# Kernel tuning notes

Hardware: AMD Instinct MI355X
Metric: run time of the kernel (lower is better)

The kernel has to match this reference:

```python
import jax, jax.numpy as jnp
import numpy as np

N_NODES = 100000
N_FEAT = 128
HIDDEN = 32
HEADS = 4
N_CLASSES = 40
N_EDGES = 1600000
NEG_SLOPE = 0.2


def gat_conv(x, src, dst, W, att_src, att_dst, bias):
    """PyG-style GATConv (concat=True, eval mode, self-loops already in src/dst).
    x: [N, Fin], W: [Fin, H*C], att_src/att_dst: [H, C], bias: [H*C].
    """
    N = x.shape[0]
    H, C = att_src.shape
    h = (x @ W).reshape(N, H, C)                       # [N, H, C]
    a_src = jnp.einsum('nhc,hc->nh', h, att_src)       # [N, H]
    a_dst = jnp.einsum('nhc,hc->nh', h, att_dst)       # [N, H]
    e = a_src[src] + a_dst[dst]                        # [E, H]
    e = jnp.where(e > 0, e, NEG_SLOPE * e)             # leaky_relu(0.2)
    # segment softmax over incoming edges of each destination node
    e_max = jax.ops.segment_max(e, dst, num_segments=N)
    e = jnp.exp(e - e_max[dst])
    denom = jax.ops.segment_sum(e, dst, num_segments=N)
    alpha = e / (denom[dst] + 1e-16)                   # [E, H]
    msg = alpha[:, :, None] * h[src]                   # [E, H, C]
    out = jax.ops.segment_sum(msg, dst, num_segments=N)  # [N, H, C]
    return out.reshape(N, H * C) + bias


def setup_inputs() -> dict:
    key = jax.random.key(0)
    ks = jax.random.split(key, 10)
    s = 0.1
    x = jax.random.normal(ks[0], (N_NODES, N_FEAT), dtype=jnp.float32)
    edge_index = jax.random.randint(ks[1], (2, N_EDGES), 0, N_NODES, dtype=jnp.int32)
    W1 = jax.random.normal(ks[2], (N_FEAT, HEADS * HIDDEN), dtype=jnp.float32) * s
    att_src1 = jax.random.normal(ks[3], (HEADS, HIDDEN), dtype=jnp.float32) * s
    att_dst1 = jax.random.normal(ks[4], (HEADS, HIDDEN), dtype=jnp.float32) * s
    b1 = jnp.zeros((HEADS * HIDDEN,), dtype=jnp.float32)
    W2 = jax.random.normal(ks[5], (HEADS * HIDDEN, HEADS * HIDDEN), dtype=jnp.float32) * s
    att_src2 = jax.random.normal(ks[6], (HEADS, HIDDEN), dtype=jnp.float32) * s
    att_dst2 = jax.random.normal(ks[7], (HEADS, HIDDEN), dtype=jnp.float32) * s
    b2 = jnp.zeros((HEADS * HIDDEN,), dtype=jnp.float32)
    Wc = jax.random.normal(ks[8], (HEADS * HIDDEN, N_CLASSES), dtype=jnp.float32) * s
    bc = jnp.zeros((N_CLASSES,), dtype=jnp.float32)
    return {"x": x, "edge_index": edge_index, "W1": W1, "att_src1": att_src1,
            "att_dst1": att_dst1, "b1": b1, "W2": W2, "att_src2": att_src2,
            "att_dst2": att_dst2, "b2": b2, "Wc": Wc, "bc": bc}


def reference(x, edge_index, W1, att_src1, att_dst1, b1, W2, att_src2, att_dst2, b2, Wc, bc):
    N = x.shape[0]
    loops = jnp.arange(N, dtype=edge_index.dtype)
    src = jnp.concatenate([edge_index[0], loops])  # PyG add_self_loops=True
    dst = jnp.concatenate([edge_index[1], loops])
    h = gat_conv(x, src, dst, W1, att_src1, att_dst1, b1)
    h = jax.nn.relu(h)  # dropout p=0.5 inactive in eval
    h = gat_conv(h, src, dst, W2, att_src2, att_dst2, b2)
    h = jax.nn.relu(h)  # dropout p=0.6 inactive in eval
    return h @ Wc + bc
```

## Files before the change

kernel.cpp:

```cpp
#include <hip/hip_runtime.h>

#define NN   100000
#define NE   1600000
#define BSH  9
#define BSZ  512
#define NBK  196
#define TA   4096
#define NBA  391
#define SCAP 64
#define CAP2 9216
#define NBG  782
#define NPREP 7

typedef _Float16 half_t;
typedef __attribute__((ext_vector_type(2))) _Float16 f16x2;
typedef __attribute__((ext_vector_type(4))) _Float16 f16x4;
typedef __attribute__((ext_vector_type(8))) _Float16 f16x8;
typedef __attribute__((ext_vector_type(4))) float    f32x4;

__global__ __launch_bounds__(256) void k_front(const float* __restrict__ X, const float* __restrict__ W1,
                                               const float* __restrict__ atts, const float* __restrict__ attd,
                                               half_t* __restrict__ H, float* __restrict__ asrc,
                                               float* __restrict__ adst,
                                               const float* __restrict__ W2, const float* __restrict__ Wc,
                                               const float* __restrict__ atts2, const float* __restrict__ attd2,
                                               half_t* __restrict__ WT2, half_t* __restrict__ WTc,
                                               const int* __restrict__ src, const int* __restrict__ dst,
                                               unsigned int* __restrict__ bpk, int* __restrict__ bh) {
  __shared__ __align__(16) char smem[21760];
  int t = threadIdx.x;
  int bid = blockIdx.x;

  if (bid >= NBG + NPREP) {
    int hb = bid - NBG - NPREP;
    int* hist  = (int*)smem;
    int* hscan = hist + NBK;
    int* cnt   = hscan + NBK;
    int* ssc   = cnt + NBK;
    unsigned int* staged = (unsigned int*)(ssc + 256);
    int e0 = hb * TA;
    if (t < NBK) { hist[t] = 0; cnt[t] = 0; }
    __syncthreads();
#pragma unroll
    for (int i = 0; i < TA / 256; i++) {
      int e = e0 + t + i * 256;
      if (e < NE) atomicAdd(&hist[dst[e] >> BSH], 1);
    }
    __syncthreads();
    {
      int v = (t < NBK) ? hist[t] : 0;
      int x = v;
      ssc[t] = x;
      for (int off = 1; off < 256; off <<= 1) {
        __syncthreads();
        int y = (t >= off) ? ssc[t - off] : 0;
        __syncthreads();
        x += y;
        ssc[t] = x;
      }
      if (t < NBK) hscan[t] = x - v;
    }
    __syncthreads();
#pragma unroll
    for (int i = 0; i < TA / 256; i++) {
      int e = e0 + t + i * 256;
      if (e < NE) {
        int d = dst[e];
        int bk = d >> BSH;
        int pos = hscan[bk] + atomicAdd(&cnt[bk], 1);
        staged[pos] = ((unsigned int)src[e] << BSH) | (unsigned int)(d & (BSZ - 1));
      }
    }
    __syncthreads();
    int wave = t >> 6, lane = t & 63;
    for (int bk = wave; bk < NBK; bk += 4) {
      int c = hist[bk];
      int cw = min(c, SCAP);
      size_t base = ((size_t)bk * NBA + hb) * SCAP;
      int lo = hscan[bk];
      for (int j = lane; j < cw; j += 64) bpk[base + j] = staged[lo + j];
      if (lane == 0) bh[bk * NBA + hb] = cw;
    }
    return;
  }

  if (bid >= NBG) {
    int b = bid - NBG;
    if (b == 6) {
      int e = t >> 5, kr = t & 31, h = e & 3;
      const float* att = ((e < 4) ? atts2 : attd2) + h * 32;
#pragma unroll
      for (int u = 0; u < 4; u++) {
        int k = u * 32 + kr;
        const float* wrow = W2 + (size_t)k * 128 + h * 32;
        float s = 0.f;
#pragma unroll
        for (int c = 0; c < 32; c += 4) {
          float4 wv = *(const float4*)(wrow + c);
          float4 av = *(const float4*)(att + c);
          s += wv.x * av.x + wv.y * av.y + wv.z * av.z + wv.w * av.w;
        }
        WT2[(size_t)(128 + e) * 128 + k] = (half_t)s;
      }
      for (int u = t; u < 8 * 128; u += 256) WT2[(size_t)136 * 128 + u] = (half_t)0.f;
      return;
    }
    float (*tile)[65] = (float(*)[65])smem;
    const float* W;
    half_t* WT;
    int k0, n0, N, NTr;
    if (b < 4) { W = W2; WT = WT2; k0 = (b >> 1) * 64; n0 = (b & 1) * 64; N = 128; NTr = 128; }
    else       { int bb = b - 4; W = Wc; WT = WTc; k0 = bb * 64; n0 = 0; N = 40; NTr = 48; }
    int col = t & 63, r4 = t >> 6;
#pragma unroll
    for (int i = 0; i < 16; i++) {
      int row = r4 * 16 + i;
      float v = 0.f;
      if (n0 + col < N) v = W[(size_t)(k0 + row) * N + n0 + col];
      tile[row][col] = v;
    }
    __syncthreads();
#pragma unroll
    for (int i = 0; i < 16; i++) {
      int nrow = r4 * 16 + i;
      if (n0 + nrow < NTr) WT[(size_t)(n0 + nrow) * 128 + k0 + col] = (half_t)tile[col][nrow];
    }
    return;
  }

  half_t* Xt = (half_t*)smem;
  half_t* Wt = Xt + 128 * 40;
  int wave = t >> 6, lane = t & 63;
  int l15 = lane & 15, quad = lane >> 4;
  int rb = bid * 128;

  for (int u = t; u < 8 * 40; u += 256) Wt[136 * 40 + u] = (half_t)0.f;

  f32x4 acc[2][9];
#pragma unroll
  for (int rt = 0; rt < 2; rt++)
#pragma unroll
    for (int ct = 0; ct < 9; ct++) acc[rt][ct] = (f32x4){0.f, 0.f, 0.f, 0.f};

  for (int k0 = 0; k0 < 128; k0 += 32) {
    __syncthreads();
#pragma unroll
    for (int i = 0; i < 4; i++) {
      int lin = i * 256 + t;
      int row = lin >> 3;
      int c4 = (lin & 7) * 4;
      float4 v = make_float4(0.f, 0.f, 0.f, 0.f);
      int gr = rb + row;
      if (gr < NN) v = *(const float4*)(X + (size_t)gr * 128 + k0 + c4);
      f16x4 hv;
      hv[0] = (half_t)v.x; hv[1] = (half_t)v.y; hv[2] = (half_t)v.z; hv[3] = (half_t)v.w;
      *(f16x4*)(Xt + row * 40 + c4) = hv;
    }
#pragma unroll
    for (int i = 0; i < 4; i++) {
      int lin = i * 256 + t;
      int kr = lin >> 5;
      int n4 = (lin & 31) * 4;
      float4 v = *(const float4*)(W1 + (size_t)(k0 + kr) * 128 + n4);
      Wt[(n4 + 0) * 40 + kr] = (half_t)v.x;
      Wt[(n4 + 1) * 40 + kr] = (half_t)v.y;
      Wt[(n4 + 2) * 40 + kr] = (half_t)v.z;
      Wt[(n4 + 3) * 40 + kr] = (half_t)v.w;
    }
    {
      int e = t >> 5, kr = t & 31, h = e & 3;
      const float* att = ((e < 4) ? atts : attd) + h * 32;
      const float* wrow = W1 + (size_t)(k0 + kr) * 128 + h * 32;
      float s = 0.f;
#pragma unroll
      for (int c = 0; c < 32; c += 4) {
        float4 wv = *(const float4*)(wrow + c);
        float4 av = *(const float4*)(att + c);
        s += wv.x * av.x + wv.y * av.y + wv.z * av.z + wv.w * av.w;
      }
      Wt[(128 + e) * 40 + kr] = (half_t)s;
    }
    __syncthreads();

    f16x8 a0 = *(const f16x8*)(Xt + (wave * 32 + l15) * 40 + quad * 8);
    f16x8 a1 = *(const f16x8*)(Xt + (wave * 32 + 16 + l15) * 40 + quad * 8);
#pragma unroll
    for (int ct = 0; ct < 9; ct++) {
      f16x8 b = *(const f16x8*)(Wt + (ct * 16 + l15) * 40 + quad * 8);
      acc[0][ct] = __builtin_amdgcn_mfma_f32_16x16x32_f16(a0, b, acc[0][ct], 0, 0, 0);
      acc[1][ct] = __builtin_amdgcn_mfma_f32_16x16x32_f16(a1, b, acc[1][ct], 0, 0, 0);
    }
  }

#pragma unroll
  for (int rt = 0; rt < 2; rt++) {
    int rbase = rb + wave * 32 + rt * 16 + quad * 4;
#pragma unroll
    for (int reg = 0; reg < 4; reg++) {
      int row = rbase + reg;
      if (row < NN) {
#pragma unroll
        for (int ct = 0; ct < 8; ct++) {
          H[(size_t)row * 128 + ct * 16 + l15] = (half_t)acc[rt][ct][reg];
        }
        if (l15 < 8) {
          float v = acc[rt][8][reg];
          if (l15 < 4) asrc[row * 4 + l15] = v;
          else         adst[row * 4 + (l15 - 4)] = v;
        }
      }
    }
  }
}

__global__ __launch_bounds__(256) void k_binB(const unsigned int* __restrict__ bpk,
                                              const int* __restrict__ bh,
                                              int* __restrict__ sbeg, int* __restrict__ send,
                                              int* __restrict__ adj) {
  __shared__ int lhist[BSZ];
  __shared__ int lscan[BSZ];
  __shared__ int lcur[BSZ];
  __shared__ int ssc[256];
  __shared__ int carr[NBA];
  __shared__ unsigned int staged[CAP2];
  int b = blockIdx.x;
  int t = threadIdx.x;
  int nbeg = b << BSH;
  int nloc = min(BSZ, NN - nbeg);
  int adjb = b * CAP2;
  for (int u = t; u < NBA; u += 256) carr[u] = bh[b * NBA + u];
  lhist[2 * t] = (2 * t < nloc) ? 1 : 0;
  lhist[2 * t + 1] = (2 * t + 1 < nloc) ? 1 : 0;
  lcur[2 * t] = 1;
  lcur[2 * t + 1] = 1;
  __syncthreads();
  int wave = t >> 6, lane = t & 63;
  for (int a = wave; a < NBA; a += 4) {
    int c = carr[a];
    size_t base = ((size_t)b * NBA + a) * SCAP;
    for (int j = lane; j < c; j += 64) atomicAdd(&lhist[bpk[base + j] & (BSZ - 1)], 1);
  }
  __syncthreads();
  {
    int v0 = lhist[2 * t], v1 = lhist[2 * t + 1];
    int s2 = v0 + v1;
    int x = s2;
    ssc[t] = x;
    for (int off = 1; off < 256; off <<= 1) {
      __syncthreads();
      int y = (t >= off) ? ssc[t - off] : 0;
      __syncthreads();
      x += y;
      ssc[t] = x;
    }
    int ex = x - s2;
    lscan[2 * t] = ex;
    lscan[2 * t + 1] = ex + v0;
  }
  __syncthreads();
  int total = lscan[BSZ - 1] + lhist[BSZ - 1];
#pragma unroll
  for (int u = 0; u < 2; u++) {
    int i = t + u * 256;
    if (i < nloc) {
      int bg = adjb + lscan[i];
      sbeg[nbeg + i] = bg;
      send[nbeg + i] = bg + lhist[i];
      staged[lscan[i]] = (unsigned int)(nbeg + i);
    }
  }
  __syncthreads();
  for (int a = wave; a < NBA; a += 4) {
    int c = carr[a];
    size_t base = ((size_t)b * NBA + a) * SCAP;
    for (int j = lane; j < c; j += 64) {
      unsigned int v = bpk[base + j];
      int dl = v & (BSZ - 1);
      int idx = lscan[dl] + atomicAdd(&lcur[dl], 1);
      if (idx < CAP2) staged[idx] = v >> BSH;
    }
  }
  __syncthreads();
  int lim = min(total, CAP2);
  for (int i = t; i < lim; i += 256) adj[adjb + i] = (int)staged[i];
}

__global__ __launch_bounds__(256) void k_agg(const half_t* __restrict__ H, const int* __restrict__ sbeg,
                                             const int* __restrict__ send, const int* __restrict__ adj,
                                             const float* __restrict__ asrc, const float* __restrict__ adst,
                                             const float* __restrict__ bias, half_t* __restrict__ out) {
  int n = blockIdx.x * 4 + (threadIdx.x >> 6);
  if (n >= NN) return;
  int lane = threadIdx.x & 63;
  int sub = lane & 7;
  int g = lane >> 3;
  int head = sub >> 1;
  float ad = adst[(size_t)n * 4 + head];
  float acc[16];
#pragma unroll
  for (int j = 0; j < 16; j++) acc[j] = 0.f;
  float wsum = 0.f;
  int beg = sbeg[n], end = send[n];
  int i = beg + g;
  int s = 0;
  float a = 0.f;
  if (i < end) {
    s = adj[i];
    a = asrc[(size_t)s * 4 + head];
  }
  while (i < end) {
    int inext = i + 8;
    int sn = 0;
    float an = 0.f;
    if (inext < end) {
      sn = adj[inext];
      an = asrc[(size_t)sn * 4 + head];
    }
    float ev = a + ad;
    ev = (ev > 0.f) ? ev : 0.2f * ev;
    float w = __expf(ev);
    const f16x8* hp = (const f16x8*)(H + (size_t)s * 128 + sub * 16);
    f16x8 h0 = hp[0], h1 = hp[1];
    wsum += w;
#pragma unroll
    for (int j = 0; j < 8; j++) acc[j] += w * (float)h0[j];
#pragma unroll
    for (int j = 0; j < 8; j++) acc[8 + j] += w * (float)h1[j];
    s = sn; a = an; i = inext;
  }
#pragma unroll
  for (int m = 8; m < 64; m <<= 1) {
    wsum += __shfl_xor(wsum, m, 64);
#pragma unroll
    for (int j = 0; j < 16; j++) acc[j] += __shfl_xor(acc[j], m, 64);
  }
  float scale = 1.0f / (wsum + 1e-16f);
  float o0 = acc[0], o1 = acc[1];
#pragma unroll
  for (int r = 1; r < 8; r++) {
    if (g == r) { o0 = acc[2 * r]; o1 = acc[2 * r + 1]; }
  }
  int ch = sub * 16 + g * 2;
  o0 = fmaxf(o0 * scale + bias[ch], 0.f);
  o1 = fmaxf(o1 * scale + bias[ch + 1], 0.f);
  f16x2 o;
  o[0] = (half_t)o0;
  o[1] = (half_t)o1;
  *(f16x2*)(out + (size_t)n * 128 + ch) = o;
}

__global__ __launch_bounds__(256) void k_gemm_att(const half_t* __restrict__ X, const half_t* __restrict__ WT,
                                                  half_t* __restrict__ H, float* __restrict__ asrc,
                                                  float* __restrict__ adst) {
  __shared__ __align__(16) half_t Xt[128 * 40];
  __shared__ __align__(16) half_t Wt[144 * 40];
  int t = threadIdx.x;
  int wave = t >> 6, lane = t & 63;
  int l15 = lane & 15, quad = lane >> 4;
  int rb = blockIdx.x * 128;

  f32x4 acc[2][9];
#pragma unroll
  for (int rt = 0; rt < 2; rt++)
#pragma unroll
    for (int ct = 0; ct < 9; ct++) acc[rt][ct] = (f32x4){0.f, 0.f, 0.f, 0.f};

  for (int k0 = 0; k0 < 128; k0 += 32) {
    __syncthreads();
#pragma unroll
    for (int i = 0; i < 2; i++) {
      int lin = i * 256 + t;
      int row = lin >> 2;
      int c8 = (lin & 3) * 8;
      f16x8 hv = (f16x8)(half_t)0;
      int gr = rb + row;
      if (gr < NN) hv = *(const f16x8*)(X + (size_t)gr * 128 + k0 + c8);
      *(f16x8*)(Xt + row * 40 + c8) = hv;
    }
#pragma unroll
    for (int i = 0; i < 3; i++) {
      int lin = i * 256 + t;
      if (lin < 576) {
        int row = lin >> 2;
        int c8 = (lin & 3) * 8;
        *(f16x8*)(Wt + row * 40 + c8) = *(const f16x8*)(WT + (size_t)row * 128 + k0 + c8);
      }
    }
    __syncthreads();

    f16x8 a0 = *(const f16x8*)(Xt + (wave * 32 + l15) * 40 + quad * 8);
    f16x8 a1 = *(const f16x8*)(Xt + (wave * 32 + 16 + l15) * 40 + quad * 8);
#pragma unroll
    for (int ct = 0; ct < 9; ct++) {
      f16x8 b = *(const f16x8*)(Wt + (ct * 16 + l15) * 40 + quad * 8);
      acc[0][ct] = __builtin_amdgcn_mfma_f32_16x16x32_f16(a0, b, acc[0][ct], 0, 0, 0);
      acc[1][ct] = __builtin_amdgcn_mfma_f32_16x16x32_f16(a1, b, acc[1][ct], 0, 0, 0);
    }
  }

#pragma unroll
  for (int rt = 0; rt < 2; rt++) {
    int rbase = rb + wave * 32 + rt * 16 + quad * 4;
#pragma unroll
    for (int reg = 0; reg < 4; reg++) {
      int row = rbase + reg;
      if (row < NN) {
#pragma unroll
        for (int ct = 0; ct < 8; ct++) {
          H[(size_t)row * 128 + ct * 16 + l15] = (half_t)acc[rt][ct][reg];
        }
        if (l15 < 8) {
          float v = acc[rt][8][reg];
          if (l15 < 4) asrc[row * 4 + l15] = v;
          else         adst[row * 4 + (l15 - 4)] = v;
        }
      }
    }
  }
}

__global__ __launch_bounds__(256) void k_classifier(const half_t* __restrict__ Hf, const half_t* __restrict__ WTc,
                                                    const float* __restrict__ bc, float* __restrict__ out) {
  __shared__ __align__(16) half_t Xt[128 * 40];
  __shared__ __align__(16) half_t Wt[48 * 40];
  int t = threadIdx.x;
  int wave = t >> 6, lane = t & 63;
  int l15 = lane & 15, quad = lane >> 4;
  int rb = blockIdx.x * 128;

  f32x4 acc[2][3];
#pragma unroll
  for (int rt = 0; rt < 2; rt++)
#pragma unroll
    for (int ct = 0; ct < 3; ct++) acc[rt][ct] = (f32x4){0.f, 0.f, 0.f, 0.f};

  for (int k0 = 0; k0 < 128; k0 += 32) {
    __syncthreads();
#pragma unroll
    for (int i = 0; i < 2; i++) {
      int lin = i * 256 + t;
      int row = lin >> 2;
      int c8 = (lin & 3) * 8;
      f16x8 hv = (f16x8)(half_t)0;
      int gr = rb + row;
      if (gr < NN) hv = *(const f16x8*)(Hf + (size_t)gr * 128 + k0 + c8);
      *(f16x8*)(Xt + row * 40 + c8) = hv;
    }
    if (t < 192) {
      int row = t >> 2;
      int c8 = (t & 3) * 8;
      *(f16x8*)(Wt + row * 40 + c8) = *(const f16x8*)(WTc + (size_t)row * 128 + k0 + c8);
    }
    __syncthreads();

    f16x8 a0 = *(const f16x8*)(Xt + (wave * 32 + l15) * 40 + quad * 8);
    f16x8 a1 = *(const f16x8*)(Xt + (wave * 32 + 16 + l15) * 40 + quad * 8);
#pragma unroll
    for (int ct = 0; ct < 3; ct++) {
      f16x8 b = *(const f16x8*)(Wt + (ct * 16 + l15) * 40 + quad * 8);
      acc[0][ct] = __builtin_amdgcn_mfma_f32_16x16x32_f16(a0, b, acc[0][ct], 0, 0, 0);
      acc[1][ct] = __builtin_amdgcn_mfma_f32_16x16x32_f16(a1, b, acc[1][ct], 0, 0, 0);
    }
  }

#pragma unroll
  for (int rt = 0; rt < 2; rt++) {
#pragma unroll
    for (int ct = 0; ct < 3; ct++) {
      int col = ct * 16 + l15;
      if (col < 40) {
        float bv = bc[col];
#pragma unroll
        for (int reg = 0; reg < 4; reg++) {
          int row = rb + wave * 32 + rt * 16 + quad * 4 + reg;
          if (row < NN) out[(size_t)row * 40 + col] = acc[rt][ct][reg] + bv;
        }
      }
    }
  }
}


extern "C" void kernel_launch(void* const* d_in, const int* in_sizes, int n_in,
                              void* d_out, int out_size, void* d_ws, size_t ws_size,
                              hipStream_t stream) {
  const float* x   = (const float*)d_in[0];
  const int*   ei  = (const int*)d_in[1];
  const float* W1  = (const float*)d_in[2];
  const float* as1 = (const float*)d_in[3];
  const float* ad1 = (const float*)d_in[4];
  const float* b1  = (const float*)d_in[5];
  const float* W2  = (const float*)d_in[6];
  const float* as2 = (const float*)d_in[7];
  const float* ad2 = (const float*)d_in[8];
  const float* b2  = (const float*)d_in[9];
  const float* Wc  = (const float*)d_in[10];
  const float* bc  = (const float*)d_in[11];
  float* out = (float*)d_out;

  const int* esrc = ei;
  const int* edst = ei + NE;

  char* w = (char*)d_ws;
  auto alloc = [&](size_t bytes) {
    void* p = (void*)w;
    w += (bytes + 255) & ~(size_t)255;
    return p;
  };
  half_t* A   = (half_t*)alloc(sizeof(half_t) * (size_t)NN * 128);
  half_t* B   = (half_t*)alloc(sizeof(half_t) * (size_t)NN * 128);
  float* asrc = (float*)alloc(sizeof(float) * (size_t)NN * 4);
  float* adst = (float*)alloc(sizeof(float) * (size_t)NN * 4);
  int* sbeg   = (int*)alloc(sizeof(int) * NN);
  int* send   = (int*)alloc(sizeof(int) * NN);
  unsigned int* bpk = (unsigned int*)alloc(sizeof(unsigned int) * (size_t)NBK * NBA * SCAP);
  int* bh     = (int*)alloc(sizeof(int) * NBK * NBA);
  int* adj    = (int*)alloc(sizeof(int) * (size_t)NBK * CAP2);
  half_t* WT2 = (half_t*)alloc(sizeof(half_t) * 144 * 128);
  half_t* WTc = (half_t*)alloc(sizeof(half_t) * 48 * 128);

  k_front<<<NBG + NPREP + NBA, 256, 0, stream>>>(x, W1, as1, ad1, A, asrc, adst,
                                                 W2, Wc, as2, ad2, WT2, WTc, esrc, edst, bpk, bh);
  k_binB<<<NBK, 256, 0, stream>>>(bpk, bh, sbeg, send, adj);

  k_agg<<<(NN + 3) / 4, 256, 0, stream>>>(A, sbeg, send, adj, asrc, adst, b1, B);

  k_gemm_att<<<(NN + 127) / 128, 256, 0, stream>>>(B, WT2, A, asrc, adst);
  k_agg<<<(NN + 3) / 4, 256, 0, stream>>>(A, sbeg, send, adj, asrc, adst, b2, B);

  k_classifier<<<(NN + 127) / 128, 256, 0, stream>>>(B, WTc, bc, out);
}
```

Before: 410.5 us.

## Rework edge binning, split weight prep kernel, and serialize aggregation per node

Moves weight transposition and attention folding for W1 into a separate small prep kernel, so the front GEMM loads pre-transposed half weights instead of recomputing them in every block. Edge binning now uses global per-bucket atomic counters with contiguous bucket regions instead of fixed per-block slots, and the second binning pass runs with 512 threads and drops the per-slot count array. The aggregation kernel changes from 8 edge groups with shuffle reductions to one wave walking edges sequentially, each lane owning two channels, with a three-deep software prefetch of indices and features. This removes the cross-lane reductions but serializes the edge loop per node, and it adds a memset and an extra kernel launch.

```diff
diff --git a/kernel.cpp b/kernel.cpp
--- a/kernel.cpp
+++ b/kernel.cpp
@@ -1,16 +1,15 @@
 #include <hip/hip_runtime.h>
 
-#define NN   100000
-#define NE   1600000
-#define BSH  9
-#define BSZ  512
-#define NBK  196
-#define TA   4096
-#define NBA  391
-#define SCAP 64
-#define CAP2 9216
-#define NBG  782
-#define NPREP 7
+#define NN    100000
+#define NE    1600000
+#define BSH   9
+#define BSZ   512
+#define NBK   196
+#define TA    8192
+#define NBA   196
+#define CAP2R 8960
+#define CAP2  9472
+#define NBG   782
 
 typedef _Float16 half_t;
 typedef __attribute__((ext_vector_type(2))) _Float16 f16x2;
@@ -18,21 +17,68 @@
 typedef __attribute__((ext_vector_type(8))) _Float16 f16x8;
 typedef __attribute__((ext_vector_type(4))) float    f32x4;
 
-__global__ __launch_bounds__(256) void k_front(const float* __restrict__ X, const float* __restrict__ W1,
-                                               const float* __restrict__ atts, const float* __restrict__ attd,
-                                               half_t* __restrict__ H, float* __restrict__ asrc,
-                                               float* __restrict__ adst,
-                                               const float* __restrict__ W2, const float* __restrict__ Wc,
-                                               const float* __restrict__ atts2, const float* __restrict__ attd2,
-                                               half_t* __restrict__ WT2, half_t* __restrict__ WTc,
-                                               const int* __restrict__ src, const int* __restrict__ dst,
-                                               unsigned int* __restrict__ bpk, int* __restrict__ bh) {
-  __shared__ __align__(16) char smem[21760];
+__global__ __launch_bounds__(256) void k_prep(const float* __restrict__ W1, const float* __restrict__ W2,
+                                              const float* __restrict__ Wc,
+                                              const float* __restrict__ as1, const float* __restrict__ ad1,
+                                              const float* __restrict__ as2, const float* __restrict__ ad2,
+                                              half_t* __restrict__ WT1, half_t* __restrict__ WT2,
+                                              half_t* __restrict__ WTc) {
+  __shared__ float tile[64][65];
+  int b = blockIdx.x, t = threadIdx.x;
+  if (b < 10) {
+    const float* W; half_t* WT; int k0, n0, N, NTr;
+    if (b < 4)      { W = W1; WT = WT1; k0 = (b >> 1) * 64; n0 = (b & 1) * 64; N = 128; NTr = 128; }
+    else if (b < 8) { int bb = b - 4; W = W2; WT = WT2; k0 = (bb >> 1) * 64; n0 = (bb & 1) * 64; N = 128; NTr = 128; }
+    else            { int bb = b - 8; W = Wc; WT = WTc; k0 = bb * 64; n0 = 0; N = 40; NTr = 48; }
+    int col = t & 63, r4 = t >> 6;
+#pragma unroll
+    for (int i = 0; i < 16; i++) {
+      int row = r4 * 16 + i;
+      float v = 0.f;
+      if (n0 + col < N) v = W[(size_t)(k0 + row) * N + n0 + col];
+      tile[row][col] = v;
+    }
+    __syncthreads();
+#pragma unroll
+    for (int i = 0; i < 16; i++) {
+      int nrow = r4 * 16 + i;
+      if (n0 + nrow < NTr) WT[(size_t)(n0 + nrow) * 128 + k0 + col] = (half_t)tile[col][nrow];
+    }
+    return;
+  }
+  const float* W  = (b == 10) ? W1 : W2;
+  const float* as = (b == 10) ? as1 : as2;
+  const float* ad = (b == 10) ? ad1 : ad2;
+  half_t* WT      = (b == 10) ? WT1 : WT2;
+  int e = t >> 5, kr = t & 31, h = e & 3;
+  const float* att = ((e < 4) ? as : ad) + h * 32;
+#pragma unroll
+  for (int u = 0; u < 4; u++) {
+    int k = u * 32 + kr;
+    const float* wrow = W + (size_t)k * 128 + h * 32;
+    float s = 0.f;
+#pragma unroll
+    for (int c = 0; c < 32; c += 4) {
+      float4 wv = *(const float4*)(wrow + c);
+      float4 av = *(const float4*)(att + c);
+      s += wv.x * av.x + wv.y * av.y + wv.z * av.z + wv.w * av.w;
+    }
+    WT[(size_t)(128 + e) * 128 + k] = (half_t)s;
+  }
+  for (int u = t; u < 8 * 128; u += 256) WT[(size_t)136 * 128 + u] = (half_t)0.f;
+}
+
+__global__ __launch_bounds__(256, 4) void k_front(const float* __restrict__ X, const half_t* __restrict__ WT1,
+                                                  half_t* __restrict__ H, float* __restrict__ asrc,
+                                                  float* __restrict__ adst,
+                                                  const int* __restrict__ src, const int* __restrict__ dst,
+                                                  unsigned int* __restrict__ bpk, int* __restrict__ gcnt) {
+  __shared__ __align__(16) char smem[36864];
   int t = threadIdx.x;
   int bid = blockIdx.x;
 
-  if (bid >= NBG + NPREP) {
-    int hb = bid - NBG - NPREP;
+  if (bid < NBA) {
+    int hb = bid;
     int* hist  = (int*)smem;
     int* hscan = hist + NBK;
     int* cnt   = hscan + NBK;
@@ -41,7 +87,6 @@
     int e0 = hb * TA;
     if (t < NBK) { hist[t] = 0; cnt[t] = 0; }
     __syncthreads();
-#pragma unroll
     for (int i = 0; i < TA / 256; i++) {
       int e = e0 + t + i * 256;
       if (e < NE) atomicAdd(&hist[dst[e] >> BSH], 1);
@@ -61,7 +106,6 @@
       if (t < NBK) hscan[t] = x - v;
     }
     __syncthreads();
-#pragma unroll
     for (int i = 0; i < TA / 256; i++) {
       int e = e0 + t + i * 256;
       if (e < NE) {
@@ -75,55 +119,14 @@
     int wave = t >> 6, lane = t & 63;
     for (int bk = wave; bk < NBK; bk += 4) {
       int c = hist[bk];
-      int cw = min(c, SCAP);
-      size_t base = ((size_t)bk * NBA + hb) * SCAP;
       int lo = hscan[bk];
-      for (int j = lane; j < cw; j += 64) bpk[base + j] = staged[lo + j];
-      if (lane == 0) bh[bk * NBA + hb] = cw;
-    }
-    return;
-  }
-
-  if (bid >= NBG) {
-    int b = bid - NBG;
-    if (b == 6) {
-      int e = t >> 5, kr = t & 31, h = e & 3;
-      const float* att = ((e < 4) ? atts2 : attd2) + h * 32;
-#pragma unroll
-      for (int u = 0; u < 4; u++) {
-        int k = u * 32 + kr;
-        const float* wrow = W2 + (size_t)k * 128 + h * 32;
-        float s = 0.f;
-#pragma unroll
-        for (int c = 0; c < 32; c += 4) {
-          float4 wv = *(const float4*)(wrow + c);
-          float4 av = *(const float4*)(att + c);
-          s += wv.x * av.x + wv.y * av.y + wv.z * av.z + wv.w * av.w;
-        }
-        WT2[(size_t)(128 + e) * 128 + k] = (half_t)s;
-      }
-      for (int u = t; u < 8 * 128; u += 256) WT2[(size_t)136 * 128 + u] = (half_t)0.f;
-      return;
-    }
-    float (*tile)[65] = (float(*)[65])smem;
-    const float* W;
-    half_t* WT;
-    int k0, n0, N, NTr;
-    if (b < 4) { W = W2; WT = WT2; k0 = (b >> 1) * 64; n0 = (b & 1) * 64; N = 128; NTr = 128; }
-    else       { int bb = b - 4; W = Wc; WT = WTc; k0 = bb * 64; n0 = 0; N = 40; NTr = 48; }
-    int col = t & 63, r4 = t >> 6;
-#pragma unroll
-    for (int i = 0; i < 16; i++) {
-      int row = r4 * 16 + i;
-      float v = 0.f;
-      if (n0 + col < N) v = W[(size_t)(k0 + row) * N + n0 + col];
-      tile[row][col] = v;
-    }
-    __syncthreads();
-#pragma unroll
-    for (int i = 0; i < 16; i++) {
-      int nrow = r4 * 16 + i;
-      if (n0 + nrow < NTr) WT[(size_t)(n0 + nrow) * 128 + k0 + col] = (half_t)tile[col][nrow];
+      int base = 0;
+      if (lane == 0 && c > 0) base = atomicAdd(&gcnt[bk], c);
+      base = __shfl(base, 0, 64);
+      int avail = CAP2R - base;
+      int cw = min(c, max(avail, 0));
+      size_t bb = (size_t)bk * CAP2R + base;
+      for (int j = lane; j < cw; j += 64) bpk[bb + j] = staged[lo + j];
     }
     return;
   }
@@ -132,9 +135,7 @@
   half_t* Wt = Xt + 128 * 40;
   int wave = t >> 6, lane = t & 63;
   int l15 = lane & 15, quad = lane >> 4;
-  int rb = bid * 128;
-
-  for (int u = t; u < 8 * 40; u += 256) Wt[136 * 40 + u] = (half_t)0.f;
+  int rb = (bid - NBA) * 128;
 
   f32x4 acc[2][9];
 #pragma unroll
@@ -157,28 +158,13 @@
       *(f16x4*)(Xt + row * 40 + c4) = hv;
     }
 #pragma unroll
-    for (int i = 0; i < 4; i++) {
+    for (int i = 0; i < 3; i++) {
       int lin = i * 256 + t;
-      int kr = lin >> 5;
-      int n4 = (lin & 31) * 4;
-      float4 v = *(const float4*)(W1 + (size_t)(k0 + kr) * 128 + n4);
-      Wt[(n4 + 0) * 40 + kr] = (half_t)v.x;
-      Wt[(n4 + 1) * 40 + kr] = (half_t)v.y;
-      Wt[(n4 + 2) * 40 + kr] = (half_t)v.z;
-      Wt[(n4 + 3) * 40 + kr] = (half_t)v.w;
-    }
-    {
-      int e = t >> 5, kr = t & 31, h = e & 3;
-      const float* att = ((e < 4) ? atts : attd) + h * 32;
-      const float* wrow = W1 + (size_t)(k0 + kr) * 128 + h * 32;
-      float s = 0.f;
-#pragma unroll
-      for (int c = 0; c < 32; c += 4) {
-        float4 wv = *(const float4*)(wrow + c);
-        float4 av = *(const float4*)(att + c);
-        s += wv.x * av.x + wv.y * av.y + wv.z * av.z + wv.w * av.w;
-      }
-      Wt[(128 + e) * 40 + kr] = (half_t)s;
+      if (lin < 576) {
+        int row = lin >> 2;
+        int c8 = (lin & 3) * 8;
+        *(f16x8*)(Wt + row * 40 + c8) = *(const f16x8*)(WT1 + (size_t)row * 128 + k0 + c8);
+      }
     }
     __syncthreads();
 
@@ -213,76 +199,58 @@
   }
 }
 
-__global__ __launch_bounds__(256) void k_binB(const unsigned int* __restrict__ bpk,
-                                              const int* __restrict__ bh,
+__global__ __launch_bounds__(512) void k_binB(const unsigned int* __restrict__ bpk,
+                                              const int* __restrict__ gcnt,
                                               int* __restrict__ sbeg, int* __restrict__ send,
                                               int* __restrict__ adj) {
   __shared__ int lhist[BSZ];
   __shared__ int lscan[BSZ];
   __shared__ int lcur[BSZ];
-  __shared__ int ssc[256];
-  __shared__ int carr[NBA];
+  __shared__ int ssc[512];
   __shared__ unsigned int staged[CAP2];
   int b = blockIdx.x;
   int t = threadIdx.x;
   int nbeg = b << BSH;
   int nloc = min(BSZ, NN - nbeg);
   int adjb = b * CAP2;
-  for (int u = t; u < NBA; u += 256) carr[u] = bh[b * NBA + u];
-  lhist[2 * t] = (2 * t < nloc) ? 1 : 0;
-  lhist[2 * t + 1] = (2 * t + 1 < nloc) ? 1 : 0;
-  lcur[2 * t] = 1;
-  lcur[2 * t + 1] = 1;
+  int cr = min(gcnt[b], CAP2R);
+  size_t rbase = (size_t)b * CAP2R;
+  lhist[t] = (t < nloc) ? 1 : 0;
+  lcur[t] = 1;
   __syncthreads();
-  int wave = t >> 6, lane = t & 63;
-  for (int a = wave; a < NBA; a += 4) {
-    int c = carr[a];
-    size_t base = ((size_t)b * NBA + a) * SCAP;
-    for (int j = lane; j < c; j += 64) atomicAdd(&lhist[bpk[base + j] & (BSZ - 1)], 1);
-  }
+  for (int j = t; j < cr; j += 512) atomicAdd(&lhist[bpk[rbase + j] & (BSZ - 1)], 1);
   __syncthreads();
   {
-    int v0 = lhist[2 * t], v1 = lhist[2 * t + 1];
-    int s2 = v0 + v1;
-    int x = s2;
+    int v = lhist[t];
+    int x = v;
     ssc[t] = x;
-    for (int off = 1; off < 256; off <<= 1) {
+    for (int off = 1; off < 512; off <<= 1) {
       __syncthreads();
       int y = (t >= off) ? ssc[t - off] : 0;
       __syncthreads();
       x += y;
       ssc[t] = x;
     }
-    int ex = x - s2;
-    lscan[2 * t] = ex;
-    lscan[2 * t + 1] = ex + v0;
+    lscan[t] = x - v;
   }
   __syncthreads();
   int total = lscan[BSZ - 1] + lhist[BSZ - 1];
-#pragma unroll
-  for (int u = 0; u < 2; u++) {
-    int i = t + u * 256;
-    if (i < nloc) {
-      int bg = adjb + lscan[i];
-      sbeg[nbeg + i] = bg;
-      send[nbeg + i] = bg + lhist[i];
-      staged[lscan[i]] = (unsigned int)(nbeg + i);
-    }
+  if (t < nloc) {
+    int bg = adjb + lscan[t];
+    sbeg[nbeg + t] = bg;
+    send[nbeg + t] = bg + lhist[t];
+    staged[lscan[t]] = (unsigned int)(nbeg + t);
   }
   __syncthreads();
-  for (int a = wave; a < NBA; a += 4) {
-    int c = carr[a];
-    size_t base = ((size_t)b * NBA + a) * SCAP;
-    for (int j = lane; j < c; j += 64) {
-      unsigned int v = bpk[base + j];
-      int dl = v & (BSZ - 1);
-      int idx = lscan[dl] + atomicAdd(&lcur[dl], 1);
-      if (idx < CAP2) staged[idx] = v >> BSH;
-    }
+  for (int j = t; j < cr; j += 512) {
+    unsigned int v = bpk[rbase + j];
+    int dl = v & (BSZ - 1);
+    int idx = lscan[dl] + atomicAdd(&lcur[dl], 1);
+    if (idx < CAP2) staged[idx] = v >> BSH;
   }
   __syncthreads();
   int lim = min(total, CAP2);
-  for (int i = t; i < lim; i += 256) adj[adjb + i] = (int)staged[i];
+  for (int i = t; i < lim; i += 512) adj[adjb + i] = (int)staged[i];
 }
 
 __global__ __launch_bounds__(256) void k_agg(const half_t* __restrict__ H, const int* __restrict__ sbeg,
@@ -292,61 +260,48 @@
   int n = blockIdx.x * 4 + (threadIdx.x >> 6);
   if (n >= NN) return;
   int lane = threadIdx.x & 63;
-  int sub = lane & 7;
-  int g = lane >> 3;
-  int head = sub >> 1;
-  float ad = adst[(size_t)n * 4 + head];
-  float acc[16];
-#pragma unroll
-  for (int j = 0; j < 16; j++) acc[j] = 0.f;
-  float wsum = 0.f;
+  int quad = lane >> 4;
+  float ad = adst[(size_t)n * 4 + quad];
+  float2 bv = *(const float2*)(bias + 2 * lane);
   int beg = sbeg[n], end = send[n];
-  int i = beg + g;
-  int s = 0;
-  float a = 0.f;
-  if (i < end) {
-    s = adj[i];
-    a = asrc[(size_t)s * 4 + head];
-  }
-  while (i < end) {
-    int inext = i + 8;
-    int sn = 0;
-    float an = 0.f;
-    if (inext < end) {
-      sn = adj[inext];
-      an = asrc[(size_t)sn * 4 + head];
-    }
-    float ev = a + ad;
-    ev = (ev > 0.f) ? ev : 0.2f * ev;
+  int last = end - 1;
+
+  float acc0 = 0.f, acc1 = 0.f, wsum = 0.f;
+
+  int j1 = (beg + 1 < end) ? beg + 1 : last;
+  int j2 = (beg + 2 < end) ? beg + 2 : last;
+  int s0 = adj[beg];
+  int sA = adj[j1];
+  int s2 = adj[j2];
+  float a0 = asrc[(size_t)s0 * 4 + quad];
+  float a1 = asrc[(size_t)sA * 4 + quad];
+  float a2 = asrc[(size_t)s2 * 4 + quad];
+  f16x2 h0 = *(const f16x2*)(H + (size_t)s0 * 128 + 2 * lane);
+  f16x2 h1 = *(const f16x2*)(H + (size_t)sA * 128 + 2 * lane);
+
+  for (int i = beg; i < end; ++i) {
+    f16x2 h2 = *(const f16x2*)(H + (size_t)s2 * 128 + 2 * lane);
+    int i3 = i + 3;
+    int j3 = (i3 < end) ? i3 : last;
+    int s3 = adj[j3];
+    float a3 = asrc[(size_t)s3 * 4 + quad];
+    float ev = a0 + ad;
+    ev = fmaxf(ev, 0.2f * ev);
     float w = __expf(ev);
-    const f16x8* hp = (const f16x8*)(H + (size_t)s * 128 + sub * 16);
-    f16x8 h0 = hp[0], h1 = hp[1];
     wsum += w;
-#pragma unroll
-    for (int j = 0; j < 8; j++) acc[j] += w * (float)h0[j];
-#pragma unroll
-    for (int j = 0; j < 8; j++) acc[8 + j] += w * (float)h1[j];
-    s = sn; a = an; i = inext;
-  }
-#pragma unroll
-  for (int m = 8; m < 64; m <<= 1) {
-    wsum += __shfl_xor(wsum, m, 64);
-#pragma unroll
-    for (int j = 0; j < 16; j++) acc[j] += __shfl_xor(acc[j], m, 64);
+    acc0 += w * (float)h0[0];
+    acc1 += w * (float)h0[1];
+    a0 = a1; a1 = a2; a2 = a3;
+    h0 = h1; h1 = h2;
+    s2 = s3;
   }
   float scale = 1.0f / (wsum + 1e-16f);
-  float o0 = acc[0], o1 = acc[1];
-#pragma unroll
-  for (int r = 1; r < 8; r++) {
-    if (g == r) { o0 = acc[2 * r]; o1 = acc[2 * r + 1]; }
-  }
-  int ch = sub * 16 + g * 2;
-  o0 = fmaxf(o0 * scale + bias[ch], 0.f);
-  o1 = fmaxf(o1 * scale + bias[ch + 1], 0.f);
+  float o0 = fmaxf(acc0 * scale + bv.x, 0.f);
+  float o1 = fmaxf(acc1 * scale + bv.y, 0.f);
   f16x2 o;
   o[0] = (half_t)o0;
   o[1] = (half_t)o1;
-  *(f16x2*)(out + (size_t)n * 128 + ch) = o;
+  *(f16x2*)(out + (size_t)n * 128 + 2 * lane) = o;
 }
 
 __global__ __launch_bounds__(256) void k_gemm_att(const half_t* __restrict__ X, const half_t* __restrict__ WT,
@@ -513,15 +468,20 @@
   float* adst = (float*)alloc(sizeof(float) * (size_t)NN * 4);
   int* sbeg   = (int*)alloc(sizeof(int) * NN);
   int* send   = (int*)alloc(sizeof(int) * NN);
-  unsigned int* bpk = (unsigned int*)alloc(sizeof(unsigned int) * (size_t)NBK * NBA * SCAP);
-  int* bh     = (int*)alloc(sizeof(int) * NBK * NBA);
+  unsigned int* bpk = (unsigned int*)alloc(sizeof(unsigned int) * (size_t)NBK * CAP2R);
+  int* gcnt   = (int*)alloc(sizeof(int) * NBK);
   int* adj    = (int*)alloc(sizeof(int) * (size_t)NBK * CAP2);
+  half_t* WT1 = (half_t*)alloc(sizeof(half_t) * 144 * 128);
   half_t* WT2 = (half_t*)alloc(sizeof(half_t) * 144 * 128);
   half_t* WTc = (half_t*)alloc(sizeof(half_t) * 48 * 128);
 
-  k_front<<<NBG + NPREP + NBA, 256, 0, stream>>>(x, W1, as1, ad1, A, asrc, adst,
-                                                 W2, Wc, as2, ad2, WT2, WTc, esrc, edst, bpk, bh);
-  k_binB<<<NBK, 256, 0, stream>>>(bpk, bh, sbeg, send, adj);
+  hipMemsetAsync(gcnt, 0, sizeof(int) * NBK, stream);
+
+  k_prep<<<12, 256, 0, stream>>>(W1, W2, Wc, as1, ad1, as2, ad2, WT1, WT2, WTc);
+
+  k_front<<<NBA + NBG, 256, 0, stream>>>(x, WT1, A, asrc, adst, esrc, edst, bpk, gcnt);
+
+  k_binB<<<NBK, 512, 0, stream>>>(bpk, gcnt, sbeg, send, adj);
 
   k_agg<<<(NN + 3) / 4, 256, 0, stream>>>(A, sbeg, send, adj, asrc, adst, b1, B);
 
```

After: 659.4 us. 1.61x slower.
